# Optimization experiments

Measured on AMD Instinct MI355X. Metric: run time of the kernel, lower is better.

## Reference

```python
import jax, jax.numpy as jnp
import numpy as np

N_NODES = 100000
D = 256
HIDDEN = 256
E = 262144


def setup_inputs() -> dict:
    key = jax.random.key(0)
    ks = jax.random.split(key, 8)
    x_src = jax.random.normal(ks[0], (N_NODES, D), dtype=jnp.float32)
    x_dst = jax.random.normal(ks[1], (N_NODES, D), dtype=jnp.float32)
    # MLP params: Linear(in_src+in_dst -> hidden), ReLU, Linear(hidden -> 1)
    W1 = jax.random.normal(ks[2], (2 * D, HIDDEN), dtype=jnp.float32) * (1.0 / np.sqrt(2 * D))
    b1 = jnp.zeros((HIDDEN,), dtype=jnp.float32)
    W2 = jax.random.normal(ks[3], (HIDDEN, 1), dtype=jnp.float32) * (1.0 / np.sqrt(HIDDEN))
    b2 = jnp.zeros((1,), dtype=jnp.float32)
    edge_index = jax.random.randint(ks[4], (2, E), 0, N_NODES, dtype=jnp.int64)
    neg_edge_index = jax.random.randint(ks[5], (2, E), 0, N_NODES, dtype=jnp.int64)
    return {"x_src": x_src, "x_dst": x_dst, "W1": W1, "b1": b1, "W2": W2,
            "b2": b2, "edge_index": edge_index, "neg_edge_index": neg_edge_index}


def _score(xs, xd, W1, b1, W2, b2):
    # MLP scorer: cat -> Linear -> ReLU -> Linear -> squeeze
    h = jnp.concatenate([xs, xd], axis=-1) @ W1 + b1   # [E, HIDDEN]
    h = jax.nn.relu(h)
    return (h @ W2 + b2).squeeze(-1)                   # [E]


def reference(x_src, x_dst, W1, b1, W2, b2, edge_index, neg_edge_index):
    src, dst = edge_index[0], edge_index[1]
    nsrc, ndst = neg_edge_index[0], neg_edge_index[1]
    pos = _score(x_src[src], x_dst[dst], W1, b1, W2, b2)
    neg = _score(x_src[nsrc], x_dst[ndst], W1, b1, W2, b2)
    return pos, neg
```

## Files before the change

kernel.cpp:

```cpp
#include <hip/hip_runtime.h>

#define D_IN   256
#define HID    256
#define NNODES 100000
#define NEDGE  262144

typedef short short8   __attribute__((ext_vector_type(8)));
typedef float float4v  __attribute__((ext_vector_type(4)));

__device__ __forceinline__ unsigned short f32_to_bf16_rne(float f) {
    unsigned int u = __float_as_uint(f);
    unsigned int r = u + 0x7FFFu + ((u >> 16) & 1u);
    return (unsigned short)(r >> 16);
}
__device__ __forceinline__ float bf16_to_f32(unsigned short h) {
    return __uint_as_float(((unsigned int)h) << 16);
}

__global__ __launch_bounds__(256) void convert_w(
    const float* __restrict__ W1, unsigned short* __restrict__ Wt)
{
    const int b = blockIdx.x;
    const int z = b >> 8, n = b & 255;
    const int k = threadIdx.x;
    const float v = W1[((size_t)(z * 256 + k)) * HID + n];
    Wt[((size_t)(z * 256 + n)) * 256 + k] = f32_to_bf16_rne(v);
}

#define SA 72

__global__ __launch_bounds__(512) void gemm_xw_mfma(
    const float* __restrict__ Xsrc, const float* __restrict__ Xdst,
    const unsigned short* __restrict__ Wt, const float* __restrict__ b1,
    unsigned short* __restrict__ U, unsigned short* __restrict__ V)
{
    const int zz = blockIdx.z;
    const float* X = zz ? Xdst : Xsrc;
    const unsigned short* Wz = Wt + (size_t)zz * 256 * 256;
    unsigned short* C = zz ? V : U;

    const int m0 = blockIdx.x * 128;

    __shared__ __align__(16) unsigned short smem[27648];
    unsigned short* As = smem;
    unsigned short* Bs = smem + 9216;

    const int t = threadIdx.x;
    const int w = t >> 6, lane = t & 63;
    const int wm = w >> 2, wn = w & 3;
    const int quad = lane >> 4, l16 = lane & 15;

    float4v acc[4][4];
#pragma unroll
    for (int mi = 0; mi < 4; mi++)
#pragma unroll
        for (int ni = 0; ni < 4; ni++) acc[mi][ni] = (float4v){0.f, 0.f, 0.f, 0.f};

    for (int ks = 0; ks < D_IN; ks += 64) {
#pragma unroll
        for (int i = 0; i < 4; i++) {
            int s = t + i * 512;
            int row = s >> 4, c4 = (s & 15) << 2;
            int gr = m0 + row; if (gr >= NNODES) gr = NNODES - 1;
            float4 a = *(const float4*)(X + (size_t)gr * D_IN + ks + c4);
            ushort4 p;
            p.x = f32_to_bf16_rne(a.x); p.y = f32_to_bf16_rne(a.y);
            p.z = f32_to_bf16_rne(a.z); p.w = f32_to_bf16_rne(a.w);
            *(ushort4*)(As + row * SA + c4) = p;
        }
#pragma unroll
        for (int i = 0; i < 4; i++) {
            int s = t + i * 512;
            int n = s >> 3, seg = s & 7;
            *(int4*)(Bs + n * SA + seg * 8) =
                *(const int4*)(Wz + (size_t)n * 256 + ks + seg * 8);
        }
        __syncthreads();
#pragma unroll
        for (int kk = 0; kk < 64; kk += 32) {
            short8 af[4], bf[4];
#pragma unroll
            for (int mi = 0; mi < 4; mi++)
                af[mi] = *(const short8*)(As + (wm * 64 + mi * 16 + l16) * SA + kk + quad * 8);
#pragma unroll
            for (int ni = 0; ni < 4; ni++)
                bf[ni] = *(const short8*)(Bs + (wn * 64 + ni * 16 + l16) * SA + kk + quad * 8);
#pragma unroll
            for (int mi = 0; mi < 4; mi++)
#pragma unroll
                for (int ni = 0; ni < 4; ni++)
                    acc[mi][ni] = __builtin_amdgcn_mfma_f32_16x16x32_bf16(
                        af[mi], bf[ni], acc[mi][ni], 0, 0, 0);
        }
        __syncthreads();
    }

    float bias[4];
#pragma unroll
    for (int ni = 0; ni < 4; ni++)
        bias[ni] = (zz == 0) ? b1[wn * 64 + ni * 16 + l16] : 0.f;

    unsigned short* Cs = smem;
#pragma unroll
    for (int h = 0; h < 2; h++) {
        if ((wn >> 1) == h) {
#pragma unroll
            for (int mi = 0; mi < 4; mi++)
#pragma unroll
                for (int ni = 0; ni < 4; ni++) {
                    int cl = (wn & 1) * 64 + ni * 16 + l16;
#pragma unroll
                    for (int r = 0; r < 4; r++) {
                        int row = wm * 64 + mi * 16 + quad * 4 + r;
                        Cs[row * 136 + cl] = f32_to_bf16_rne(acc[mi][ni][r] + bias[ni]);
                    }
                }
        }
        __syncthreads();
#pragma unroll
        for (int i = 0; i < 4; i++) {
            int s = t + i * 512;
            int row = s >> 4, seg = s & 15;
            int gr = m0 + row;
            if (gr < NNODES)
                *(int4*)(C + (size_t)gr * HID + h * 128 + seg * 8) =
                    *(const int4*)(Cs + row * 136 + seg * 8);
        }
        __syncthreads();
    }
}

__global__ __launch_bounds__(256) void edge_score_bf16(
    const unsigned short* __restrict__ U, const unsigned short* __restrict__ V,
    const float* __restrict__ W2, const float* __restrict__ b2,
    const int* __restrict__ epos, const int* __restrict__ eneg,
    float* __restrict__ out)
{
    const int w = threadIdx.x >> 6, lane = threadIdx.x & 63;
    const int ebase = blockIdx.x * 16 + w * 4;

    const float4 w2 = *(const float4*)(W2 + lane * 4);

    const int* ei = (ebase < NEDGE) ? epos : eneg;
    const int eb2 = (ebase < NEDGE) ? ebase : ebase - NEDGE;

    int sidx[4], didx[4];
#pragma unroll
    for (int j = 0; j < 4; j++) {
        sidx[j] = ei[eb2 + j];
        didx[j] = ei[NEDGE + eb2 + j];
    }
    ushort4 uu[4], vv[4];
#pragma unroll
    for (int j = 0; j < 4; j++) {
        uu[j] = *(const ushort4*)(U + (size_t)sidx[j] * HID + lane * 4);
        vv[j] = *(const ushort4*)(V + (size_t)didx[j] * HID + lane * 4);
    }
    const float bb2 = b2[0];
#pragma unroll
    for (int j = 0; j < 4; j++) {
        float p = fmaxf(bf16_to_f32(uu[j].x) + bf16_to_f32(vv[j].x), 0.f) * w2.x
                + fmaxf(bf16_to_f32(uu[j].y) + bf16_to_f32(vv[j].y), 0.f) * w2.y
                + fmaxf(bf16_to_f32(uu[j].z) + bf16_to_f32(vv[j].z), 0.f) * w2.z
                + fmaxf(bf16_to_f32(uu[j].w) + bf16_to_f32(vv[j].w), 0.f) * w2.w;
#pragma unroll
        for (int off = 32; off; off >>= 1)
            p += __shfl_down(p, off, 64);
        if (lane == 0) out[ebase + j] = p + bb2;
    }
}

__global__ __launch_bounds__(256) void edge_score_direct(
    const float* __restrict__ xs_, const float* __restrict__ xd_,
    const float* __restrict__ W1, const float* __restrict__ b1,
    const float* __restrict__ W2, const float* __restrict__ b2,
    const int* __restrict__ epos, const int* __restrict__ eneg,
    float* __restrict__ out)
{
    __shared__ float xrow[2 * D_IN];
    __shared__ float red[256];
    const int e = blockIdx.x;
    const int* ei = (e < NEDGE) ? epos : eneg;
    const int e2  = (e < NEDGE) ? e : e - NEDGE;
    const int s = ei[e2];
    const int d = ei[NEDGE + e2];
    const int t = threadIdx.x;

    xrow[t]        = xs_[(size_t)s * D_IN + t];
    xrow[D_IN + t] = xd_[(size_t)d * D_IN + t];
    __syncthreads();

    float acc = b1[t];
    for (int k = 0; k < 2 * D_IN; k++)
        acc += xrow[k] * W1[(size_t)k * HID + t];
    acc = fmaxf(acc, 0.f);
    red[t] = acc * W2[t];
    __syncthreads();
    for (int st = 128; st; st >>= 1) {
        if (t < st) red[t] += red[t + st];
        __syncthreads();
    }
    if (t == 0) out[e] = red[0] + b2[0];
}

extern "C" void kernel_launch(void* const* d_in, const int* in_sizes, int n_in,
                              void* d_out, int out_size, void* d_ws, size_t ws_size,
                              hipStream_t stream) {
    const float* x_src = (const float*)d_in[0];
    const float* x_dst = (const float*)d_in[1];
    const float* W1    = (const float*)d_in[2];
    const float* b1    = (const float*)d_in[3];
    const float* W2    = (const float*)d_in[4];
    const float* b2    = (const float*)d_in[5];
    const int*   epos  = (const int*)d_in[6];
    const int*   eneg  = (const int*)d_in[7];
    float* out = (float*)d_out;

    const size_t uv   = (size_t)NNODES * HID;
    const size_t need = (2 * uv + 2 * 256 * 256) * sizeof(unsigned short);
    if (ws_size >= need) {
        unsigned short* U  = (unsigned short*)d_ws;
        unsigned short* V  = U + uv;
        unsigned short* Wt = V + uv;
        convert_w<<<512, 256, 0, stream>>>(W1, Wt);
        dim3 g1((NNODES + 127) / 128, 1, 2);
        gemm_xw_mfma<<<g1, 512, 0, stream>>>(x_src, x_dst, Wt, b1, U, V);
        edge_score_bf16<<<(2 * NEDGE) / 16, 256, 0, stream>>>(U, V, W2, b2, epos, eneg, out);
    } else {
        edge_score_direct<<<2 * NEDGE, 256, 0, stream>>>(x_src, x_dst, W1, b1, W2, b2, epos, eneg, out);
    }
}
```

Baseline: 337.8 us.

## Prefetch GEMM tiles into registers, tile W transpose, batch more edges per warp

```diff
diff --git a/kernel.cpp b/kernel.cpp
--- a/kernel.cpp
+++ b/kernel.cpp
@@ -20,11 +20,21 @@
 __global__ __launch_bounds__(256) void convert_w(
     const float* __restrict__ W1, unsigned short* __restrict__ Wt)
 {
-    const int b = blockIdx.x;
-    const int z = b >> 8, n = b & 255;
-    const int k = threadIdx.x;
-    const float v = W1[((size_t)(z * 256 + k)) * HID + n];
-    Wt[((size_t)(z * 256 + n)) * 256 + k] = f32_to_bf16_rne(v);
+    __shared__ float tile[64][65];
+    const int z = blockIdx.z, kb = blockIdx.x * 64, nb = blockIdx.y * 64;
+    const int t = threadIdx.x;
+    const int g = t >> 6, c = t & 63;
+#pragma unroll
+    for (int r = 0; r < 16; r++) {
+        int kl = g * 16 + r;
+        tile[kl][c] = W1[((size_t)(z * 256 + kb + kl)) * 256 + nb + c];
+    }
+    __syncthreads();
+#pragma unroll
+    for (int r = 0; r < 16; r++) {
+        int nl = g * 16 + r;
+        Wt[((size_t)(z * 256 + nb + nl)) * 256 + kb + c] = f32_to_bf16_rne(tile[c][nl]);
+    }
 }
 
 #define SA 72
@@ -50,32 +60,49 @@
     const int wm = w >> 2, wn = w & 3;
     const int quad = lane >> 4, l16 = lane & 15;
 
+    int arow[4], ac4[4], brow[4], bseg[4];
+    const float* agp[4];
+#pragma unroll
+    for (int i = 0; i < 4; i++) {
+        int s = t + i * 512;
+        arow[i] = s >> 4; ac4[i] = (s & 15) << 2;
+        int gr = m0 + arow[i]; if (gr >= NNODES) gr = NNODES - 1;
+        agp[i] = X + (size_t)gr * D_IN + ac4[i];
+        brow[i] = s >> 3; bseg[i] = (s & 7) << 3;
+    }
+
     float4v acc[4][4];
 #pragma unroll
     for (int mi = 0; mi < 4; mi++)
 #pragma unroll
         for (int ni = 0; ni < 4; ni++) acc[mi][ni] = (float4v){0.f, 0.f, 0.f, 0.f};
 
+    float4 aReg[4]; int4 bReg[4];
+#pragma unroll
+    for (int i = 0; i < 4; i++) {
+        aReg[i] = *(const float4*)(agp[i]);
+        bReg[i] = *(const int4*)(Wz + (size_t)brow[i] * 256 + bseg[i]);
+    }
+
     for (int ks = 0; ks < D_IN; ks += 64) {
 #pragma unroll
         for (int i = 0; i < 4; i++) {
-            int s = t + i * 512;
-            int row = s >> 4, c4 = (s & 15) << 2;
-            int gr = m0 + row; if (gr >= NNODES) gr = NNODES - 1;
-            float4 a = *(const float4*)(X + (size_t)gr * D_IN + ks + c4);
             ushort4 p;
-            p.x = f32_to_bf16_rne(a.x); p.y = f32_to_bf16_rne(a.y);
-            p.z = f32_to_bf16_rne(a.z); p.w = f32_to_bf16_rne(a.w);
-            *(ushort4*)(As + row * SA + c4) = p;
-        }
-#pragma unroll
-        for (int i = 0; i < 4; i++) {
-            int s = t + i * 512;
-            int n = s >> 3, seg = s & 7;
-            *(int4*)(Bs + n * SA + seg * 8) =
-                *(const int4*)(Wz + (size_t)n * 256 + ks + seg * 8);
-        }
-        __syncthreads();
+            p.x = f32_to_bf16_rne(aReg[i].x); p.y = f32_to_bf16_rne(aReg[i].y);
+            p.z = f32_to_bf16_rne(aReg[i].z); p.w = f32_to_bf16_rne(aReg[i].w);
+            *(ushort4*)(As + arow[i] * SA + ac4[i]) = p;
+            *(int4*)(Bs + brow[i] * SA + bseg[i]) = bReg[i];
+        }
+        __syncthreads();
+
+        if (ks < 192) {
+#pragma unroll
+            for (int i = 0; i < 4; i++) {
+                aReg[i] = *(const float4*)(agp[i] + ks + 64);
+                bReg[i] = *(const int4*)(Wz + (size_t)brow[i] * 256 + ks + 64 + bseg[i]);
+            }
+        }
+
 #pragma unroll
         for (int kk = 0; kk < 64; kk += 32) {
             short8 af[4], bf[4];
@@ -137,28 +164,28 @@
     float* __restrict__ out)
 {
     const int w = threadIdx.x >> 6, lane = threadIdx.x & 63;
-    const int ebase = blockIdx.x * 16 + w * 4;
+    const int ebase = blockIdx.x * 32 + w * 8;
 
     const float4 w2 = *(const float4*)(W2 + lane * 4);
 
     const int* ei = (ebase < NEDGE) ? epos : eneg;
     const int eb2 = (ebase < NEDGE) ? ebase : ebase - NEDGE;
 
-    int sidx[4], didx[4];
-#pragma unroll
-    for (int j = 0; j < 4; j++) {
+    int sidx[8], didx[8];
+#pragma unroll
+    for (int j = 0; j < 8; j++) {
         sidx[j] = ei[eb2 + j];
         didx[j] = ei[NEDGE + eb2 + j];
     }
-    ushort4 uu[4], vv[4];
-#pragma unroll
-    for (int j = 0; j < 4; j++) {
+    ushort4 uu[8], vv[8];
+#pragma unroll
+    for (int j = 0; j < 8; j++) {
         uu[j] = *(const ushort4*)(U + (size_t)sidx[j] * HID + lane * 4);
         vv[j] = *(const ushort4*)(V + (size_t)didx[j] * HID + lane * 4);
     }
     const float bb2 = b2[0];
 #pragma unroll
-    for (int j = 0; j < 4; j++) {
+    for (int j = 0; j < 8; j++) {
         float p = fmaxf(bf16_to_f32(uu[j].x) + bf16_to_f32(vv[j].x), 0.f) * w2.x
                 + fmaxf(bf16_to_f32(uu[j].y) + bf16_to_f32(vv[j].y), 0.f) * w2.y
                 + fmaxf(bf16_to_f32(uu[j].z) + bf16_to_f32(vv[j].z), 0.f) * w2.z
@@ -222,10 +249,10 @@
         unsigned short* U  = (unsigned short*)d_ws;
         unsigned short* V  = U + uv;
         unsigned short* Wt = V + uv;
-        convert_w<<<512, 256, 0, stream>>>(W1, Wt);
+        convert_w<<<dim3(4, 4, 2), 256, 0, stream>>>(W1, Wt);
         dim3 g1((NNODES + 127) / 128, 1, 2);
         gemm_xw_mfma<<<g1, 512, 0, stream>>>(x_src, x_dst, Wt, b1, U, V);
-        edge_score_bf16<<<(2 * NEDGE) / 16, 256, 0, stream>>>(U, V, W2, b2, epos, eneg, out);
+        edge_score_bf16<<<(2 * NEDGE) / 32, 256, 0, stream>>>(U, V, W2, b2, epos, eneg, out);
     } else {
         edge_score_direct<<<2 * NEDGE, 256, 0, stream>>>(x_src, x_dst, W1, b1, W2, b2, epos, eneg, out);
     }
```

Result: slower. 371.2 us (+9.9%).
